# Kernel optimization log

Hardware: AMD Instinct MI355X
Metric: run time of the kernel (lower is better)

The kernel has to match this reference:

```python
import jax, jax.numpy as jnp
import numpy as np

B, S, D = 2, 2048, 2048
QC, KVC = 16, 4          # query heads, kv heads (GQA)
HD = D // QC             # head_dim = 128
FF = 8192                # ff_dim = 4 * model_dim
EPS = 1e-5


def rotate_every_two(x):
    x1 = x[..., ::2]
    x2 = x[..., 1::2]
    return jnp.stack((-x2, x1), axis=-1).reshape(*x.shape[:-1], -1)


def apply_rope(x, seq_len, sin, cos):
    sin = sin[:seq_len]
    cos = cos[:seq_len]
    return x * cos + rotate_every_two(x) * sin


def rmsnorm(x, w, eps=EPS):
    xf = x.astype(jnp.float32)
    xf = xf * jax.lax.rsqrt(jnp.square(xf).mean(-1, keepdims=True) + eps)
    return xf.astype(x.dtype) * w


def attention(x, mask, sin, cos, wqkv, wo):
    b, s, d = x.shape
    kv_repeat = QC // KVC
    qkv = x @ wqkv
    q = qkv[..., :D].reshape(b, s, kv_repeat, KVC, HD)
    q = jnp.moveaxis(q, 1, 3)                       # (b, rep, kvc, s, hd)
    q = apply_rope(q, s, sin, cos)
    k, v = jnp.split(qkv[..., D:], 2, axis=-1)
    k = k.reshape(b, s, KVC, HD).swapaxes(1, 2)     # (b, kvc, s, hd)
    v = v.reshape(b, s, KVC, HD).swapaxes(1, 2)
    k = apply_rope(k, s, sin, cos) * (HD ** -0.5)
    k = k[:, None]                                  # (b, 1, kvc, s, hd)
    v = v[:, None]
    a = q @ k.swapaxes(-2, -1)                      # (b, rep, kvc, s, s)
    a = a + mask[:s, :s]
    a = jax.nn.softmax(a, axis=-1)
    o = a @ v                                       # (b, rep, kvc, s, hd)
    o = o.reshape(b, QC, s, HD).swapaxes(1, 2).reshape(b, s, d)
    return o @ wo


def ffn(x, wk, wv):
    k = jnp.square(jax.nn.relu(x @ wk))
    return k @ wv


def setup_inputs() -> dict:
    key = jax.random.key(0)
    ks = jax.random.split(key, 6)
    std = 0.02
    x = jax.random.normal(ks[0], (B, S, D), jnp.float32)
    wqkv = std * jax.random.normal(ks[1], (D, D + 2 * KVC * HD), jnp.float32)
    wo = std * jax.random.normal(ks[2], (D, D), jnp.float32)
    ffn_wk = std * jax.random.normal(ks[3], (D, FF), jnp.float32)
    ffn_wv = std * jax.random.normal(ks[4], (FF, D), jnp.float32)
    norm1_w = jnp.ones((D,), jnp.float32)
    norm2_w = jnp.ones((D,), jnp.float32)
    # GPT-J style interleaved RoPE tables of shape (S, HD)
    pos = jnp.arange(S, dtype=jnp.float32)
    inv_freq = 1.0 / (10000.0 ** (jnp.arange(0, HD, 2, dtype=jnp.float32) / HD))
    freqs = pos[:, None] * inv_freq[None, :]
    rope_sin = jnp.repeat(jnp.sin(freqs), 2, axis=-1)
    rope_cos = jnp.repeat(jnp.cos(freqs), 2, axis=-1)
    # additive causal mask
    mask = jnp.where(jnp.tril(jnp.ones((S, S), bool)), 0.0, -1e9).astype(jnp.float32)
    return dict(x=x, mask=mask, rope_sin=rope_sin, rope_cos=rope_cos,
                wqkv=wqkv, wo=wo, norm1_w=norm1_w, norm2_w=norm2_w,
                ffn_wk=ffn_wk, ffn_wv=ffn_wv)


def reference(x, mask, rope_sin, rope_cos, wqkv, wo, norm1_w, norm2_w, ffn_wk, ffn_wv):
    # pre-norm residual block
    x = x + attention(rmsnorm(x, norm1_w), mask, rope_sin, rope_cos, wqkv, wo)
    x = x + ffn(rmsnorm(x, norm2_w), ffn_wk, ffn_wv)
    return x
```

## Files before the change

### kernel.cpp

```cpp
#include <hip/hip_runtime.h>
#include <hip/hip_bf16.h>
#include <cstdint>
#include <cstddef>
#include <type_traits>

typedef __hip_bfloat16 bf16;
typedef float f32x4 __attribute__((ext_vector_type(4)));
typedef short s16x8 __attribute__((ext_vector_type(8)));

#define BB 2
#define SS 2048
#define DD 2048
#define QCH 16
#define KVH 4
#define HD 128
#define FF 8192

__device__ __forceinline__ float b2f(bf16 v) { return __bfloat162float(v); }
__device__ __forceinline__ bf16 f2b(float v) { return __float2bfloat16(v); }

__device__ __forceinline__ void gl_lds16(const void* g, void* l) {
    __builtin_amdgcn_global_load_lds((const __attribute__((address_space(1))) void*)g,
                                     (__attribute__((address_space(3))) void*)l,
                                     16, 0, 0);
}

#define GBAR __builtin_amdgcn_s_barrier()
#define LGK0 do { asm volatile("s_waitcnt lgkmcnt(0)" ::: "memory"); __builtin_amdgcn_sched_barrier(0); } while (0)

__global__ __launch_bounds__(256) void transpose_cast(const float* __restrict__ src,
                                                      bf16* __restrict__ dst,
                                                      int K, int N) {
    __shared__ float t[32][33];
    int n0 = blockIdx.x * 32, k0 = blockIdx.y * 32;
    int tx = threadIdx.x, ty = threadIdx.y;
#pragma unroll
    for (int j = 0; j < 4; ++j)
        t[ty + j * 8][tx] = src[(size_t)(k0 + ty + j * 8) * N + n0 + tx];
    __syncthreads();
#pragma unroll
    for (int j = 0; j < 4; ++j)
        dst[(size_t)(n0 + ty + j * 8) * K + k0 + tx] = f2b(t[tx][ty + j * 8]);
}

__global__ __launch_bounds__(256) void rmsnorm_k(const float* __restrict__ x,
                                                 const float* __restrict__ w,
                                                 bf16* __restrict__ out) {
    int row = blockIdx.x;
    int tid = threadIdx.x;
    const float* xr = x + (size_t)row * DD + tid * 8;
    f32x4 a0 = *(const f32x4*)xr;
    f32x4 a1 = *(const f32x4*)(xr + 4);
    float f[8];
    float ss = 0.f;
#pragma unroll
    for (int i = 0; i < 4; ++i) { f[i] = a0[i]; f[i + 4] = a1[i]; }
#pragma unroll
    for (int i = 0; i < 8; ++i) ss += f[i] * f[i];
#pragma unroll
    for (int off = 32; off > 0; off >>= 1) ss += __shfl_down(ss, off);
    __shared__ float red[4];
    int lane = tid & 63, wv_ = tid >> 6;
    if (lane == 0) red[wv_] = ss;
    __syncthreads();
    float tot = red[0] + red[1] + red[2] + red[3];
    float scale = rsqrtf(tot * (1.0f / DD) + 1e-5f);
#pragma unroll
    for (int i = 0; i < 8; ++i) {
        int col = tid * 8 + i;
        out[(size_t)row * DD + col] = f2b(f[i] * scale * w[col]);
    }
}

__global__ __launch_bounds__(256) void rope_scatter(const bf16* __restrict__ qkv,
                                                    const float* __restrict__ rsin,
                                                    const float* __restrict__ rcos,
                                                    bf16* __restrict__ q_r,
                                                    bf16* __restrict__ k_r,
                                                    bf16* __restrict__ v_t) {
    int p = blockIdx.x * 256 + threadIdx.x;
    int row = p / 1536;
    int c2 = p - row * 1536;
    int col = c2 * 2;
    int b = row >> 11, s = row & 2047;
    size_t qbase = (size_t)row * 3072 + col;
    float e = b2f(qkv[qbase]);
    float o = b2f(qkv[qbase + 1]);
    if (col < 2048) {
        int h = col >> 7, hd = col & 127;
        float cs = rcos[s * HD + hd];
        float sn = rsin[s * HD + hd];
        size_t base = (((size_t)(b * QCH + h)) * SS + s) * HD + hd;
        q_r[base]     = f2b(e * cs - o * sn);
        q_r[base + 1] = f2b(o * cs + e * sn);
    } else if (col < 2560) {
        int cc = col - 2048;
        int kc = cc >> 7, hd = cc & 127;
        float cs = rcos[s * HD + hd];
        float sn = rsin[s * HD + hd];
        const float kscale = 0.08838834764831845f;
        size_t base = (((size_t)(b * KVH + kc)) * SS + s) * HD + hd;
        k_r[base]     = f2b((e * cs - o * sn) * kscale);
        k_r[base + 1] = f2b((o * cs + e * sn) * kscale);
    } else {
        int cc = col - 2560;
        int kc = cc >> 7, hd = cc & 127;
        size_t base = (((size_t)(b * KVH + kc)) * HD + hd) * SS + s;
        v_t[base]      = qkv[qbase];
        v_t[base + SS] = qkv[qbase + 1];
    }
}

template <int MREP, int EPI, typename CT>
__global__ __launch_bounds__(512, 2) void gemm256(const bf16* __restrict__ A,
                                                  const bf16* __restrict__ Bt,
                                                  const float* __restrict__ res,
                                                  CT* __restrict__ C,
                                                  int M, int N, int K) {
    static_assert(MREP == 4 || MREP == 8, "MREP");
    constexpr int MH  = MREP / 2;
    constexpr int NJA = MREP / 4;
    constexpr int BM  = MREP * 32;

    __shared__ __align__(16) bf16 As[2][2][MREP * 1024];
    __shared__ __align__(16) bf16 Bs[2][2][8192];

    const int tid = threadIdx.x;
    const int w = tid >> 6, lane = tid & 63;
    const int lm = lane & 15, quad = lane >> 4;
    const int wm = w >> 2, wn = w & 3;

    const int cpx = gridDim.x >> 3;
    const int sb = (blockIdx.x & 7) * cpx + (blockIdx.x >> 3);
    const int nbx = N >> 8;
    const int bx = sb % nbx, by = sb / nbx;
    const int m0 = by * BM, n0 = bx * 256;

    const size_t K2 = (size_t)K * 2;
    const int srow = tid >> 3;
    const int sboff = ((tid & 7) ^ (srow & 7)) * 16;
    const int NT = K >> 6;

    const char* Abase = (const char*)A + (size_t)m0 * K2 + sboff;
    const char* Bbase = (const char*)Bt + (size_t)n0 * K2 + sboff;
    char* lAs = (char*)&As[0][0][0];
    char* lBs = (char*)&Bs[0][0][0];
    constexpr int ASZ = MREP * 2048;

    auto stA = [&](int db, int h, int t) {
#pragma unroll
        for (int j = 0; j < NJA; ++j) {
            int row = h * (MREP * 16) + j * 64 + srow;
            gl_lds16(Abase + (size_t)row * K2 + (size_t)t * 128,
                     lAs + (db * 2 + h) * ASZ + j * 8192 + tid * 16);
        }
    };
    auto stB = [&](int db, int h, int t) {
#pragma unroll
        for (int j = 0; j < 2; ++j) {
            int row = h * 128 + j * 64 + srow;
            gl_lds16(Bbase + (size_t)row * K2 + (size_t)t * 128,
                     lBs + (db * 2 + h) * 16384 + j * 8192 + tid * 16);
        }
    };

    const int c0 = (quad ^ (lm & 7)) * 16;
    const int c1 = ((4 + quad) ^ (lm & 7)) * 16;

    s16x8 a0[MH][2], a1[MH][2], b0[2][2], b1[2][2];
    f32x4 acc[MREP][4];
    const f32x4 zero = {0.f, 0.f, 0.f, 0.f};
#pragma unroll
    for (int i = 0; i < MREP; ++i)
#pragma unroll
        for (int j = 0; j < 4; ++j) acc[i][j] = zero;

    auto ldA = [&](s16x8 (&a)[MH][2], int db, int mh) {
        const char* base = lAs + (db * 2 + wm) * ASZ + (mh * (MH * 16) + lm) * 128;
#pragma unroll
        for (int mi = 0; mi < MH; ++mi) {
            a[mi][0] = *(const s16x8*)(base + mi * 2048 + c0);
            a[mi][1] = *(const s16x8*)(base + mi * 2048 + c1);
        }
    };
    auto ldB = [&](s16x8 (&b)[2][2], int db, int nh) {
        const char* base = lBs + (db * 2 + (wn >> 1)) * 16384 + ((wn & 1) * 64 + nh * 32 + lm) * 128;
#pragma unroll
        for (int ni = 0; ni < 2; ++ni) {
            b[ni][0] = *(const s16x8*)(base + ni * 2048 + c0);
            b[ni][1] = *(const s16x8*)(base + ni * 2048 + c1);
        }
    };
    auto mm = [&](s16x8 (&a)[MH][2], s16x8 (&b)[2][2], int mh, int nh) {
#pragma unroll
        for (int mi = 0; mi < MH; ++mi)
#pragma unroll
            for (int ni = 0; ni < 2; ++ni)
#pragma unroll
                for (int kk = 0; kk < 2; ++kk)
                    acc[mh * MH + mi][nh * 2 + ni] = __builtin_amdgcn_mfma_f32_16x16x32_bf16(
                        a[mi][kk], b[ni][kk], acc[mh * MH + mi][nh * 2 + ni], 0, 0, 0);
    };

    stA(0, 0, 0); stA(0, 1, 0); stB(0, 0, 0); stB(0, 1, 0);
    stA(1, 0, 1); stA(1, 1, 1);
    if constexpr (NJA == 2) asm volatile("s_waitcnt vmcnt(4)" ::: "memory");
    else                    asm volatile("s_waitcnt vmcnt(2)" ::: "memory");
    GBAR;

    const int NI = NT >> 1;
#pragma unroll 1
    for (int i = 0; i < NI; ++i) {
        const int t1 = 2 * i + 1;
        int tA = 2 * i + 2; if (tA >= NT) tA = 0;
        int tB = 2 * i + 3; if (tB >= NT) tB = 0;
        ldA(a0, 0, 0); ldB(b0, 0, 0); stB(1, 0, t1);
        GBAR; LGK0;
        __builtin_amdgcn_s_setprio(1); mm(a0, b0, 0, 0); __builtin_amdgcn_s_setprio(0);
        GBAR;
        ldA(a1, 0, 1); ldB(b1, 0, 1); stB(1, 1, t1);
        GBAR; LGK0;
        __builtin_amdgcn_s_setprio(1); mm(a1, b1, 1, 1); __builtin_amdgcn_s_setprio(0);
        GBAR;
        stA(0, 0, tA);
        GBAR; LGK0;
        __builtin_amdgcn_s_setprio(1); mm(a0, b1, 0, 1); __builtin_amdgcn_s_setprio(0);
        GBAR;
        stA(0, 1, tA);
        GBAR; LGK0;
        __builtin_amdgcn_s_setprio(1); mm(a1, b0, 1, 0); __builtin_amdgcn_s_setprio(0);
        if constexpr (NJA == 2) asm volatile("s_waitcnt vmcnt(4)" ::: "memory");
        else                    asm volatile("s_waitcnt vmcnt(2)" ::: "memory");
        GBAR;
        ldA(a0, 1, 0); ldB(b0, 1, 0); stB(0, 0, tA);
        GBAR; LGK0;
        __builtin_amdgcn_s_setprio(1); mm(a0, b0, 0, 0); __builtin_amdgcn_s_setprio(0);
        GBAR;
        ldA(a1, 1, 1); ldB(b1, 1, 1); stB(0, 1, tA);
        GBAR; LGK0;
        __builtin_amdgcn_s_setprio(1); mm(a1, b1, 1, 1); __builtin_amdgcn_s_setprio(0);
        GBAR;
        stA(1, 0, tB);
        GBAR; LGK0;
        __builtin_amdgcn_s_setprio(1); mm(a0, b1, 0, 1); __builtin_amdgcn_s_setprio(0);
        GBAR;
        stA(1, 1, tB);
        GBAR; LGK0;
        __builtin_amdgcn_s_setprio(1); mm(a1, b0, 1, 0); __builtin_amdgcn_s_setprio(0);
        if constexpr (NJA == 2) asm volatile("s_waitcnt vmcnt(4)" ::: "memory");
        else                    asm volatile("s_waitcnt vmcnt(2)" ::: "memory");
        GBAR;
    }

#pragma unroll
    for (int mi = 0; mi < MREP; ++mi)
#pragma unroll
        for (int ni = 0; ni < 4; ++ni) {
            int gr = m0 + wm * (MREP * 16) + mi * 16 + quad * 4;
            int gc = n0 + wn * 64 + ni * 16 + lm;
#pragma unroll
            for (int r = 0; r < 4; ++r) {
                size_t idx = (size_t)(gr + r) * N + gc;
                float v = acc[mi][ni][r];
                if (EPI == 1) v += res[idx];
                if (EPI == 2) { v = fmaxf(v, 0.f); v = v * v; }
                if constexpr (std::is_same<CT, float>::value) C[idx] = v;
                else C[idx] = f2b(v);
            }
        }
}

__global__ __launch_bounds__(256) void attn_k(const bf16* __restrict__ q_r,
                                              const bf16* __restrict__ k_r,
                                              const bf16* __restrict__ v_t,
                                              bf16* __restrict__ o_buf) {
    __shared__ __align__(16) bf16 Ks[64 * 128];
    __shared__ __align__(16) bf16 Vs[128 * 64];
    __shared__ __align__(16) bf16 Ps[4][32 * 72];
    const int i = blockIdx.x;
    const int qt = i >> 5, hb = i & 31;
    const int h = hb & 15, b = hb >> 4;
    const int tid = threadIdx.x, w = tid >> 6, lane = tid & 63;
    const int lm = lane & 15, quad = lane >> 4;
    const int kvh = h & (KVH - 1);
    const int qw0 = qt * 128 + w * 32;
    bf16* Pw = &Ps[w][0];

    s16x8 aq[2][4];
#pragma unroll
    for (int mt = 0; mt < 2; ++mt) {
        const bf16* qp = q_r + (((size_t)(b * QCH + h)) * SS + qw0 + mt * 16 + lm) * HD + quad * 8;
#pragma unroll
        for (int c = 0; c < 4; ++c) aq[mt][c] = *(const s16x8*)(qp + c * 32);
    }

    const char* kbase = (const char*)(k_r + ((size_t)(b * KVH + kvh)) * SS * HD);
    const char* vbase = (const char*)(v_t + ((size_t)(b * KVH + kvh)) * HD * SS);

    const int krow = tid >> 4, kslot = tid & 15;
    const int ksrc_off = ((kslot ^ (krow & 15)) * 16);
    const int vrow = tid >> 3, vslot = tid & 7;

    const f32x4 zero = {0.f, 0.f, 0.f, 0.f};
    f32x4 accO[2][8];
#pragma unroll
    for (int mt = 0; mt < 2; ++mt)
#pragma unroll
        for (int ni = 0; ni < 8; ++ni) accO[mt][ni] = zero;
    float lp[2][4] = {{0.f, 0.f, 0.f, 0.f}, {0.f, 0.f, 0.f, 0.f}};

    const int ntiles = 2 * qt + 2;
    for (int kt = 0; kt < ntiles; ++kt) {
        const int kb = kt * 64;
#pragma unroll
        for (int j = 0; j < 4; ++j) {
            int kr = krow + j * 16;
            gl_lds16(kbase + (size_t)(kb + kr) * 256 + ksrc_off, (char*)Ks + tid * 16 + j * 4096);
        }
#pragma unroll
        for (int j = 0; j < 4; ++j) {
            int vr = vrow + j * 32;
            gl_lds16(vbase + (size_t)vr * (SS * 2) + kb * 2 + ((vslot ^ (vr & 7)) * 16),
                     (char*)Vs + tid * 16 + j * 4096);
        }
        __syncthreads();

        const bool active = (kb <= qw0 + 31);
        if (active) {
#pragma unroll
            for (int nt = 0; nt < 4; ++nt) {
                const int krl = nt * 16 + lm;
                s16x8 kf[4];
#pragma unroll
                for (int c = 0; c < 4; ++c)
                    kf[c] = *(const s16x8*)((char*)Ks + krl * 256 + (((c * 4 + quad) ^ lm) * 16));
                const int colk = kb + krl;
#pragma unroll
                for (int mt = 0; mt < 2; ++mt) {
                    f32x4 sc = zero;
#pragma unroll
                    for (int c = 0; c < 4; ++c)
                        sc = __builtin_amdgcn_mfma_f32_16x16x32_bf16(aq[mt][c], kf[c], sc, 0, 0, 0);
#pragma unroll
                    for (int r = 0; r < 4; ++r) {
                        int rowq = qw0 + mt * 16 + quad * 4 + r;
                        float p = (colk <= rowq) ? __expf(sc[r]) : 0.f;
                        lp[mt][r] += p;
                        Pw[(mt * 16 + quad * 4 + r) * 72 + nt * 16 + lm] = f2b(p);
                    }
                }
            }
            s16x8 pf[2][2];
#pragma unroll
            for (int mt = 0; mt < 2; ++mt)
#pragma unroll
                for (int kf2 = 0; kf2 < 2; ++kf2)
                    pf[mt][kf2] = *(const s16x8*)&Pw[(mt * 16 + lm) * 72 + kf2 * 32 + quad * 8];
#pragma unroll
            for (int ni = 0; ni < 8; ++ni) {
                const int vrl = ni * 16 + lm;
#pragma unroll
                for (int kf2 = 0; kf2 < 2; ++kf2) {
                    s16x8 vf = *(const s16x8*)((char*)Vs + vrl * 128 + (((kf2 * 4 + quad) ^ (lm & 7)) * 16));
#pragma unroll
                    for (int mt = 0; mt < 2; ++mt)
                        accO[mt][ni] = __builtin_amdgcn_mfma_f32_16x16x32_bf16(pf[mt][kf2], vf, accO[mt][ni], 0, 0, 0);
                }
            }
        }
        __syncthreads();
    }

#pragma unroll
    for (int mt = 0; mt < 2; ++mt)
#pragma unroll
        for (int r = 0; r < 4; ++r) {
            float l = lp[mt][r];
#pragma unroll
            for (int off = 1; off < 16; off <<= 1) l += __shfl_xor(l, off);
            lp[mt][r] = 1.f / l;
        }

#pragma unroll
    for (int mt = 0; mt < 2; ++mt)
#pragma unroll
        for (int ni = 0; ni < 8; ++ni)
#pragma unroll
            for (int r = 0; r < 4; ++r) {
                int s = qw0 + mt * 16 + quad * 4 + r;
                size_t idx = ((size_t)(b * SS + s)) * DD + h * HD + ni * 16 + lm;
                o_buf[idx] = f2b(accO[mt][ni][r] * lp[mt][r]);
            }
}

extern "C" void kernel_launch(void* const* d_in, const int* in_sizes, int n_in,
                              void* d_out, int out_size, void* d_ws, size_t ws_size,
                              hipStream_t stream) {
    const float* x    = (const float*)d_in[0];
    const float* rsin = (const float*)d_in[2];
    const float* rcos = (const float*)d_in[3];
    const float* wqkv = (const float*)d_in[4];
    const float* wo   = (const float*)d_in[5];
    const float* n1w  = (const float*)d_in[6];
    const float* n2w  = (const float*)d_in[7];
    const float* wk   = (const float*)d_in[8];
    const float* wv   = (const float*)d_in[9];
    float* out = (float*)d_out;

    char* ws = (char*)d_ws;
    size_t off = 0;
    auto allocb = [&](size_t elems) { bf16* p = (bf16*)(ws + off); off += elems * 2; return p; };
    auto allocf = [&](size_t elems) { float* p = (float*)(ws + off); off += elems * 4; return p; };
    bf16* wqkvT = allocb((size_t)3072 * 2048);
    bf16* woT   = allocb((size_t)2048 * 2048);
    bf16* wkT   = allocb((size_t)8192 * 2048);
    bf16* wvT   = allocb((size_t)2048 * 8192);
    bf16* xn    = allocb((size_t)4096 * 2048);
    bf16* qkv   = allocb((size_t)4096 * 3072);
    bf16* q_r   = allocb((size_t)BB * QCH * SS * HD);
    bf16* k_r   = allocb((size_t)BB * KVH * SS * HD);
    bf16* v_t   = allocb((size_t)BB * KVH * HD * SS);
    bf16* ffnh  = allocb((size_t)4096 * 8192);
    float* x1   = allocf((size_t)4096 * 2048);

    dim3 tb(32, 8);
    transpose_cast<<<dim3(3072 / 32, 2048 / 32), tb, 0, stream>>>(wqkv, wqkvT, 2048, 3072);
    transpose_cast<<<dim3(2048 / 32, 2048 / 32), tb, 0, stream>>>(wo, woT, 2048, 2048);
    transpose_cast<<<dim3(8192 / 32, 2048 / 32), tb, 0, stream>>>(wk, wkT, 2048, 8192);
    transpose_cast<<<dim3(2048 / 32, 8192 / 32), tb, 0, stream>>>(wv, wvT, 8192, 2048);

    rmsnorm_k<<<4096, 256, 0, stream>>>(x, n1w, xn);
    gemm256<8, 0, bf16><<<192, 512, 0, stream>>>(xn, wqkvT, nullptr, qkv, 4096, 3072, 2048);
    rope_scatter<<<(4096 * 1536) / 256, 256, 0, stream>>>(qkv, rsin, rcos, q_r, k_r, v_t);
    attn_k<<<512, 256, 0, stream>>>(q_r, k_r, v_t, qkv );
    gemm256<4, 1, float><<<256, 512, 0, stream>>>(qkv, woT, x, x1, 4096, 2048, 2048);
    rmsnorm_k<<<4096, 256, 0, stream>>>(x1, n2w, xn);
    gemm256<8, 2, bf16><<<512, 512, 0, stream>>>(xn, wkT, nullptr, ffnh, 4096, 8192, 2048);
    gemm256<4, 1, float><<<256, 512, 0, stream>>>(ffnh, wvT, x1, out, 4096, 2048, 8192);
}
```

Before: 883.1 us.

## Split-K the N=2048 GEMMs into 256x256 tiles with fused residual-add kernels

The two output projections (wo and FFN down) now use 256x256 tiles with a 2-way split over K instead of 128x256 tiles, so 256 blocks still fill the device while each block gets more reuse per tile. The partial sums go to scratch buffers (reusing ffnh and qkv), and new kernels add the partials plus the residual, one of them fused with the second rmsnorm. The GEMM pipeline is also reordered to prefetch both A and B for the next stage together, waiting with vmcnt(8). The cost is extra fp32 partial traffic and an added elementwise pass.

```diff
diff --git a/kernel.cpp b/kernel.cpp
--- a/kernel.cpp
+++ b/kernel.cpp
@@ -27,6 +27,7 @@
 
 #define GBAR __builtin_amdgcn_s_barrier()
 #define LGK0 do { asm volatile("s_waitcnt lgkmcnt(0)" ::: "memory"); __builtin_amdgcn_sched_barrier(0); } while (0)
+#define VM8  asm volatile("s_waitcnt vmcnt(8)" ::: "memory")
 
 __global__ __launch_bounds__(256) void transpose_cast(const float* __restrict__ src,
                                                       bf16* __restrict__ dst,
@@ -69,6 +70,59 @@
     for (int i = 0; i < 8; ++i) {
         int col = tid * 8 + i;
         out[(size_t)row * DD + col] = f2b(f[i] * scale * w[col]);
+    }
+}
+
+__global__ __launch_bounds__(256) void rmsnorm_add3(const float* __restrict__ pa,
+                                                    const float* __restrict__ pb,
+                                                    const float* __restrict__ xr,
+                                                    const float* __restrict__ w,
+                                                    float* __restrict__ x1,
+                                                    bf16* __restrict__ out) {
+    int row = blockIdx.x;
+    int tid = threadIdx.x;
+    size_t base = (size_t)row * DD + tid * 8;
+    f32x4 a0 = *(const f32x4*)(pa + base);
+    f32x4 a1 = *(const f32x4*)(pa + base + 4);
+    f32x4 b0 = *(const f32x4*)(pb + base);
+    f32x4 b1 = *(const f32x4*)(pb + base + 4);
+    f32x4 c0 = *(const f32x4*)(xr + base);
+    f32x4 c1 = *(const f32x4*)(xr + base + 4);
+    a0 = a0 + b0 + c0;
+    a1 = a1 + b1 + c1;
+    *(f32x4*)(x1 + base) = a0;
+    *(f32x4*)(x1 + base + 4) = a1;
+    float f[8];
+    float ss = 0.f;
+#pragma unroll
+    for (int i = 0; i < 4; ++i) { f[i] = a0[i]; f[i + 4] = a1[i]; }
+#pragma unroll
+    for (int i = 0; i < 8; ++i) ss += f[i] * f[i];
+#pragma unroll
+    for (int off = 32; off > 0; off >>= 1) ss += __shfl_down(ss, off);
+    __shared__ float red[4];
+    int lane = tid & 63, wv_ = tid >> 6;
+    if (lane == 0) red[wv_] = ss;
+    __syncthreads();
+    float tot = red[0] + red[1] + red[2] + red[3];
+    float scale = rsqrtf(tot * (1.0f / DD) + 1e-5f);
+#pragma unroll
+    for (int i = 0; i < 8; ++i) {
+        int col = tid * 8 + i;
+        out[base + i] = f2b(f[i] * scale * w[col]);
+    }
+}
+
+__global__ __launch_bounds__(256) void add3_k(const float* __restrict__ pa,
+                                              const float* __restrict__ pb,
+                                              const float* __restrict__ x1,
+                                              float* __restrict__ o, int n4) {
+    int stride = gridDim.x * 256;
+    for (int i = blockIdx.x * 256 + threadIdx.x; i < n4; i += stride) {
+        f32x4 a = ((const f32x4*)pa)[i];
+        f32x4 b = ((const f32x4*)pb)[i];
+        f32x4 c = ((const f32x4*)x1)[i];
+        ((f32x4*)o)[i] = a + b + c;
     }
 }
 
@@ -111,18 +165,14 @@
     }
 }
 
-template <int MREP, int EPI, typename CT>
-__global__ __launch_bounds__(512, 2) void gemm256(const bf16* __restrict__ A,
-                                                  const bf16* __restrict__ Bt,
-                                                  const float* __restrict__ res,
-                                                  CT* __restrict__ C,
-                                                  int M, int N, int K) {
-    static_assert(MREP == 4 || MREP == 8, "MREP");
-    constexpr int MH  = MREP / 2;
-    constexpr int NJA = MREP / 4;
-    constexpr int BM  = MREP * 32;
-
-    __shared__ __align__(16) bf16 As[2][2][MREP * 1024];
+template <int EPI, typename CT>
+__global__ __launch_bounds__(512) void gemm256(const bf16* __restrict__ A,
+                                               const bf16* __restrict__ Bt,
+                                               CT* __restrict__ C,
+                                               CT* __restrict__ Cp,
+                                               int M, int N, int KH, int ldk,
+                                               int nsplit) {
+    __shared__ __align__(16) bf16 As[2][2][8192];
     __shared__ __align__(16) bf16 Bs[2][2][8192];
 
     const int tid = threadIdx.x;
@@ -131,35 +181,38 @@
     const int wm = w >> 2, wn = w & 3;
 
     const int cpx = gridDim.x >> 3;
-    const int sb = (blockIdx.x & 7) * cpx + (blockIdx.x >> 3);
+    int sb = (blockIdx.x & 7) * cpx + (blockIdx.x >> 3);
     const int nbx = N >> 8;
+    const int ntiles = (M >> 8) * nbx;
+    const int kh = (nsplit == 2 && sb >= ntiles) ? 1 : 0;
+    sb -= kh * ntiles;
     const int bx = sb % nbx, by = sb / nbx;
-    const int m0 = by * BM, n0 = bx * 256;
-
-    const size_t K2 = (size_t)K * 2;
+    const int m0 = by * 256, n0 = bx * 256;
+    CT* Cw = kh ? Cp : C;
+
+    const size_t LD2 = (size_t)ldk * 2;
     const int srow = tid >> 3;
     const int sboff = ((tid & 7) ^ (srow & 7)) * 16;
-    const int NT = K >> 6;
-
-    const char* Abase = (const char*)A + (size_t)m0 * K2 + sboff;
-    const char* Bbase = (const char*)Bt + (size_t)n0 * K2 + sboff;
+    const int NT = KH >> 6;
+
+    const char* Abase = (const char*)A + (size_t)m0 * LD2 + (size_t)kh * KH * 2 + sboff;
+    const char* Bbase = (const char*)Bt + (size_t)n0 * LD2 + (size_t)kh * KH * 2 + sboff;
     char* lAs = (char*)&As[0][0][0];
     char* lBs = (char*)&Bs[0][0][0];
-    constexpr int ASZ = MREP * 2048;
 
     auto stA = [&](int db, int h, int t) {
 #pragma unroll
-        for (int j = 0; j < NJA; ++j) {
-            int row = h * (MREP * 16) + j * 64 + srow;
-            gl_lds16(Abase + (size_t)row * K2 + (size_t)t * 128,
-                     lAs + (db * 2 + h) * ASZ + j * 8192 + tid * 16);
+        for (int j = 0; j < 2; ++j) {
+            int row = h * 128 + j * 64 + srow;
+            gl_lds16(Abase + (size_t)row * LD2 + (size_t)t * 128,
+                     lAs + (db * 2 + h) * 16384 + j * 8192 + tid * 16);
         }
     };
     auto stB = [&](int db, int h, int t) {
 #pragma unroll
         for (int j = 0; j < 2; ++j) {
             int row = h * 128 + j * 64 + srow;
-            gl_lds16(Bbase + (size_t)row * K2 + (size_t)t * 128,
+            gl_lds16(Bbase + (size_t)row * LD2 + (size_t)t * 128,
                      lBs + (db * 2 + h) * 16384 + j * 8192 + tid * 16);
         }
     };
@@ -167,18 +220,18 @@
     const int c0 = (quad ^ (lm & 7)) * 16;
     const int c1 = ((4 + quad) ^ (lm & 7)) * 16;
 
-    s16x8 a0[MH][2], a1[MH][2], b0[2][2], b1[2][2];
-    f32x4 acc[MREP][4];
+    s16x8 a0[4][2], a1[4][2], b0[2][2], b1[2][2];
+    f32x4 acc[8][4];
     const f32x4 zero = {0.f, 0.f, 0.f, 0.f};
 #pragma unroll
-    for (int i = 0; i < MREP; ++i)
+    for (int i = 0; i < 8; ++i)
 #pragma unroll
         for (int j = 0; j < 4; ++j) acc[i][j] = zero;
 
-    auto ldA = [&](s16x8 (&a)[MH][2], int db, int mh) {
-        const char* base = lAs + (db * 2 + wm) * ASZ + (mh * (MH * 16) + lm) * 128;
-#pragma unroll
-        for (int mi = 0; mi < MH; ++mi) {
+    auto ldA = [&](s16x8 (&a)[4][2], int db, int mh) {
+        const char* base = lAs + (db * 2 + wm) * 16384 + (mh * 64 + lm) * 128;
+#pragma unroll
+        for (int mi = 0; mi < 4; ++mi) {
             a[mi][0] = *(const s16x8*)(base + mi * 2048 + c0);
             a[mi][1] = *(const s16x8*)(base + mi * 2048 + c1);
         }
@@ -191,81 +244,76 @@
             b[ni][1] = *(const s16x8*)(base + ni * 2048 + c1);
         }
     };
-    auto mm = [&](s16x8 (&a)[MH][2], s16x8 (&b)[2][2], int mh, int nh) {
-#pragma unroll
-        for (int mi = 0; mi < MH; ++mi)
+    auto mm = [&](s16x8 (&a)[4][2], s16x8 (&b)[2][2], int mh, int nh) {
+#pragma unroll
+        for (int mi = 0; mi < 4; ++mi)
 #pragma unroll
             for (int ni = 0; ni < 2; ++ni)
 #pragma unroll
                 for (int kk = 0; kk < 2; ++kk)
-                    acc[mh * MH + mi][nh * 2 + ni] = __builtin_amdgcn_mfma_f32_16x16x32_bf16(
-                        a[mi][kk], b[ni][kk], acc[mh * MH + mi][nh * 2 + ni], 0, 0, 0);
+                    acc[mh * 4 + mi][nh * 2 + ni] = __builtin_amdgcn_mfma_f32_16x16x32_bf16(
+                        a[mi][kk], b[ni][kk], acc[mh * 4 + mi][nh * 2 + ni], 0, 0, 0);
     };
 
     stA(0, 0, 0); stA(0, 1, 0); stB(0, 0, 0); stB(0, 1, 0);
-    stA(1, 0, 1); stA(1, 1, 1);
-    if constexpr (NJA == 2) asm volatile("s_waitcnt vmcnt(4)" ::: "memory");
-    else                    asm volatile("s_waitcnt vmcnt(2)" ::: "memory");
+    stA(1, 0, 1); stA(1, 1, 1); stB(1, 0, 1); stB(1, 1, 1);
+    VM8;
     GBAR;
 
     const int NI = NT >> 1;
 #pragma unroll 1
     for (int i = 0; i < NI; ++i) {
-        const int t1 = 2 * i + 1;
         int tA = 2 * i + 2; if (tA >= NT) tA = 0;
         int tB = 2 * i + 3; if (tB >= NT) tB = 0;
-        ldA(a0, 0, 0); ldB(b0, 0, 0); stB(1, 0, t1);
+        ldA(a0, 0, 0); ldB(b0, 0, 0);
         GBAR; LGK0;
         __builtin_amdgcn_s_setprio(1); mm(a0, b0, 0, 0); __builtin_amdgcn_s_setprio(0);
         GBAR;
-        ldA(a1, 0, 1); ldB(b1, 0, 1); stB(1, 1, t1);
+        ldA(a1, 0, 1); ldB(b1, 0, 1);
         GBAR; LGK0;
         __builtin_amdgcn_s_setprio(1); mm(a1, b1, 1, 1); __builtin_amdgcn_s_setprio(0);
         GBAR;
-        stA(0, 0, tA);
-        GBAR; LGK0;
+        stA(0, 0, tA); stA(0, 1, tA);
+        GBAR;
         __builtin_amdgcn_s_setprio(1); mm(a0, b1, 0, 1); __builtin_amdgcn_s_setprio(0);
         GBAR;
-        stA(0, 1, tA);
-        GBAR; LGK0;
+        stB(0, 0, tA); stB(0, 1, tA);
+        GBAR;
         __builtin_amdgcn_s_setprio(1); mm(a1, b0, 1, 0); __builtin_amdgcn_s_setprio(0);
-        if constexpr (NJA == 2) asm volatile("s_waitcnt vmcnt(4)" ::: "memory");
-        else                    asm volatile("s_waitcnt vmcnt(2)" ::: "memory");
-        GBAR;
-        ldA(a0, 1, 0); ldB(b0, 1, 0); stB(0, 0, tA);
+        VM8;
+        GBAR;
+        ldA(a0, 1, 0); ldB(b0, 1, 0);
         GBAR; LGK0;
         __builtin_amdgcn_s_setprio(1); mm(a0, b0, 0, 0); __builtin_amdgcn_s_setprio(0);
         GBAR;
-        ldA(a1, 1, 1); ldB(b1, 1, 1); stB(0, 1, tA);
+        ldA(a1, 1, 1); ldB(b1, 1, 1);
         GBAR; LGK0;
         __builtin_amdgcn_s_setprio(1); mm(a1, b1, 1, 1); __builtin_amdgcn_s_setprio(0);
         GBAR;
-        stA(1, 0, tB);
-        GBAR; LGK0;
+        stA(1, 0, tB); stA(1, 1, tB);
+        GBAR;
         __builtin_amdgcn_s_setprio(1); mm(a0, b1, 0, 1); __builtin_amdgcn_s_setprio(0);
         GBAR;
-        stA(1, 1, tB);
-        GBAR; LGK0;
+        stB(1, 0, tB); stB(1, 1, tB);
+        GBAR;
         __builtin_amdgcn_s_setprio(1); mm(a1, b0, 1, 0); __builtin_amdgcn_s_setprio(0);
-        if constexpr (NJA == 2) asm volatile("s_waitcnt vmcnt(4)" ::: "memory");
-        else                    asm volatile("s_waitcnt vmcnt(2)" ::: "memory");
-        GBAR;
-    }
-
-#pragma unroll
-    for (int mi = 0; mi < MREP; ++mi)
+        VM8;
+        GBAR;
+    }
+
+#pragma unroll
+    for (int mi = 0; mi < 8; ++mi)
 #pragma unroll
         for (int ni = 0; ni < 4; ++ni) {
-            int gr = m0 + wm * (MREP * 16) + mi * 16 + quad * 4;
+            int gr = m0 + wm * 128 + mi * 16 + quad * 4;
             int gc = n0 + wn * 64 + ni * 16 + lm;
 #pragma unroll
             for (int r = 0; r < 4; ++r) {
                 size_t idx = (size_t)(gr + r) * N + gc;
                 float v = acc[mi][ni][r];
-                if (EPI == 1) v += res[idx];
                 if (EPI == 2) { v = fmaxf(v, 0.f); v = v * v; }
-                if constexpr (std::is_same<CT, float>::value) C[idx] = v;
-                else C[idx] = f2b(v);
+                if constexpr (std::is_same<CT, float>::value) Cw[idx] = v;
+                else Cw[idx] = f2b(v);
             }
         }
 }
@@ -422,6 +470,8 @@
     bf16* v_t   = allocb((size_t)BB * KVH * HD * SS);
     bf16* ffnh  = allocb((size_t)4096 * 8192);
     float* x1   = allocf((size_t)4096 * 2048);
+    float* pwo = (float*)ffnh;
+    float* pdn = (float*)qkv;
 
     dim3 tb(32, 8);
     transpose_cast<<<dim3(3072 / 32, 2048 / 32), tb, 0, stream>>>(wqkv, wqkvT, 2048, 3072);
@@ -430,11 +480,12 @@
     transpose_cast<<<dim3(2048 / 32, 8192 / 32), tb, 0, stream>>>(wv, wvT, 8192, 2048);
 
     rmsnorm_k<<<4096, 256, 0, stream>>>(x, n1w, xn);
-    gemm256<8, 0, bf16><<<192, 512, 0, stream>>>(xn, wqkvT, nullptr, qkv, 4096, 3072, 2048);
+    gemm256<0, bf16><<<192, 512, 0, stream>>>(xn, wqkvT, qkv, qkv, 4096, 3072, 2048, 2048, 1);
     rope_scatter<<<(4096 * 1536) / 256, 256, 0, stream>>>(qkv, rsin, rcos, q_r, k_r, v_t);
     attn_k<<<512, 256, 0, stream>>>(q_r, k_r, v_t, qkv );
-    gemm256<4, 1, float><<<256, 512, 0, stream>>>(qkv, woT, x, x1, 4096, 2048, 2048);
-    rmsnorm_k<<<4096, 256, 0, stream>>>(x1, n2w, xn);
-    gemm256<8, 2, bf16><<<512, 512, 0, stream>>>(xn, wkT, nullptr, ffnh, 4096, 8192, 2048);
-    gemm256<4, 1, float><<<256, 512, 0, stream>>>(ffnh, wvT, x1, out, 4096, 2048, 8192);
-}
+    gemm256<0, float><<<256, 512, 0, stream>>>(qkv, woT, x1, pwo, 4096, 2048, 1024, 2048, 2);
+    rmsnorm_add3<<<4096, 256, 0, stream>>>(x1, pwo, x, n2w, x1, xn);
+    gemm256<2, bf16><<<512, 512, 0, stream>>>(xn, wkT, ffnh, ffnh, 4096, 8192, 2048, 2048, 1);
+    gemm256<0, float><<<256, 512, 0, stream>>>(ffnh, wvT, out, pdn, 4096, 2048, 4096, 8192, 2);
+    add3_k<<<2048, 256, 0, stream>>>(out, pdn, x1, out, (4096 * 2048) / 4);
+}
```

Result: faster. 811.8 us (-8.1%).
